# Kernel tuning notes

Measured on AMD Instinct MI355X. Metric: run time of the kernel, lower is better.

Reference implementation:

```python
import jax, jax.numpy as jnp
import numpy as np

B, N, K = 8, 2048, 16   # batch, points, neighbors (after dropping self)
EPS = 1e-5


def _bn(y, g, b, m, v):
    # eval-mode batchnorm over channel dim 1, y: [B,C,...]
    sh = (1, -1) + (1,) * (y.ndim - 2)
    inv = g.reshape(sh) / jnp.sqrt(v.reshape(sh) + EPS)
    return (y - m.reshape(sh)) * inv + b.reshape(sh)


def setup_inputs() -> dict:
    key = jax.random.key(0)
    ks = jax.random.split(key, 16)
    d = {}
    d["x"] = jax.random.normal(ks[0], (B, 3, N), dtype=jnp.float32)
    # pre: Conv1d(3->24, k=1) + BN
    d["w_pre"] = jax.random.normal(ks[1], (24, 3), dtype=jnp.float32) * 0.3
    d["b_pre"] = jax.random.normal(ks[2], (24,), dtype=jnp.float32) * 0.1
    d["g_pre"] = 1.0 + 0.1 * jax.random.normal(ks[3], (24,), dtype=jnp.float32)
    d["be_pre"] = 0.1 * jax.random.normal(ks[4], (24,), dtype=jnp.float32)
    d["m_pre"] = 0.1 * jax.random.normal(ks[5], (24,), dtype=jnp.float32)
    d["v_pre"] = jax.random.uniform(ks[6], (24,), minval=0.5, maxval=1.5, dtype=jnp.float32)
    # shared_mlp_1: Conv2d(48->12, 1, bias=False) + BN
    d["w1"] = jax.random.normal(ks[7], (12, 48), dtype=jnp.float32) * 0.15
    d["g1"] = 1.0 + 0.1 * jax.random.normal(ks[8], (12,), dtype=jnp.float32)
    d["be1"] = 0.1 * jax.random.normal(ks[9], (12,), dtype=jnp.float32)
    d["m1"] = 0.1 * jax.random.normal(ks[10], (12,), dtype=jnp.float32)
    d["v1"] = jax.random.uniform(ks[11], (12,), minval=0.5, maxval=1.5, dtype=jnp.float32)
    # shared_mlp_2: Conv2d(60->12, 1, bias=False) + BN
    d["w2"] = jax.random.normal(ks[12], (12, 60), dtype=jnp.float32) * 0.15
    d["g2"] = 1.0 + 0.1 * jax.random.normal(ks[13], (12,), dtype=jnp.float32)
    d["be2"] = 0.1 * jax.random.normal(ks[14], (12,), dtype=jnp.float32)
    d["m2"] = 0.1 * jax.random.normal(ks[15], (12,), dtype=jnp.float32)
    d["v2"] = jnp.ones((12,), dtype=jnp.float32)
    # shared_mlp_3: Conv2d(72->12, 1, bias=False), no BN
    d["w3"] = jax.random.normal(jax.random.fold_in(key, 99), (12, 72), dtype=jnp.float32) * 0.15
    return d


def reference(x, w_pre, b_pre, g_pre, be_pre, m_pre, v_pre,
              w1, g1, be1, m1, v1, w2, g2, be2, m2, v2, w3):
    # pre: 1x1 conv1d + BN + ReLU -> [B,24,N]
    pre = jnp.einsum('oc,bcn->bon', w_pre, x) + b_pre[None, :, None]
    pre = jax.nn.relu(_bn(pre, g_pre, be_pre, m_pre, v_pre))

    # kNN on xyz = x.detach(): [B,N,3]
    pts = jax.lax.stop_gradient(jnp.swapaxes(x, 1, 2))
    sq = jnp.sum(pts * pts, axis=-1)                              # [B,N]
    d2 = sq[:, :, None] + sq[:, None, :] - 2.0 * jnp.einsum('bnc,bmc->bnm', pts, pts)
    _, idx = jax.lax.top_k(-d2, K + 1)                             # nearest K+1 incl. self
    idx = idx[..., 1:]                                             # drop self -> [B,N,K]

    # gather neighbor features: [B,24,N,K]
    grouped = jax.vmap(lambda f, i: f[:, i])(pre, idx)
    center = jnp.broadcast_to(pre[..., None], grouped.shape)
    y = jnp.concatenate([center, grouped], axis=1)                 # [B,48,N,K]

    h1 = jax.nn.relu(_bn(jnp.einsum('oc,bcnk->bonk', w1, y), g1, be1, m1, v1))
    y = jnp.concatenate([h1, y], axis=1)                           # [B,60,N,K]
    h2 = jax.nn.relu(_bn(jnp.einsum('oc,bcnk->bonk', w2, y), g2, be2, m2, v2))
    y = jnp.concatenate([h2, y], axis=1)                           # [B,72,N,K]
    h3 = jnp.einsum('oc,bcnk->bonk', w3, y)
    y = jnp.concatenate([h3, y], axis=1)                           # [B,84,N,K]

    y = jnp.max(y, axis=-1)                                        # maxpool over neighbors -> [B,84,N]
    return jnp.concatenate([y, x], axis=1)                         # [B,87,N]
```

## Files before the change

kernel.cpp:

```cpp
#include <hip/hip_runtime.h>
#include <math.h>

#define EPS 1e-5f
#define NBATCH 8
#define NPTS 2048
#define KNB 16
#define BIG 3.2e38f

#define CHUNK_PTS 32
#define KNN_BLKS (NBATCH * 64)
#define THREADS 1024
#define FUSED_LDS 65536

#define WS_PRE 0
#define WS_AUX (16384 * 24)
#define WS_IDX (WS_AUX + 16384 * 72)

__device__ __forceinline__ float dist2f(float mex, float mey, float mez,
                                        float sqn, float4 q) {
  float dot2 = fmaf(mex, q.x, fmaf(mey, q.y, __fmul_rn(mez, q.z)));
  return __fsub_rn(__fadd_rn(sqn, q.w), dot2);
}

__global__ __launch_bounds__(THREADS, 8) void fused_kernel(
    const float* __restrict__ x,
    const float* __restrict__ w_pre, const float* __restrict__ b_pre,
    const float* __restrict__ g_pre, const float* __restrict__ be_pre,
    const float* __restrict__ m_pre, const float* __restrict__ v_pre,
    const float* __restrict__ w1, const float* __restrict__ g1,
    const float* __restrict__ be1, const float* __restrict__ m1,
    const float* __restrict__ v1,
    const float* __restrict__ w2, const float* __restrict__ g2,
    const float* __restrict__ be2, const float* __restrict__ m2,
    const float* __restrict__ v2, const float* __restrict__ w3,
    float* __restrict__ pre, float* __restrict__ aux,
    int* __restrict__ knn_out) {
  extern __shared__ char smem[];
  float4* C4   = (float4*)smem;
  float* slist = (float*)(smem + 32768);
  float* fwp   = slist;
  float* fbp   = fwp + 72;
  float* fw1t  = fbp + 24;
  float* fb1   = fw1t + 576;
  float* fw2t  = fb1 + 12;
  float* fb2   = fw2t + 720;
  float* fw3t  = fb2 + 12;
  float* sinv1 = fw3t + 576;
  float* sinv2 = sinv1 + 12;
  float* sinvP = sinv2 + 12;
  float* sd2  = slist;
  int*   sidx = (int*)(slist + 640);
  int*   scnt = (int*)(slist + 1280);

  int tid = threadIdx.x;
  int bi = blockIdx.x;
  int b = bi >> 6, chunk = bi & 63;
  const float* xb = x + (size_t)b * 3 * NPTS;

  for (int j = tid; j < NPTS; j += THREADS) {
    float xx = xb[j], yy = xb[NPTS + j], zz = xb[2 * NPTS + j];
    float sq = __fadd_rn(__fadd_rn(__fmul_rn(xx, xx), __fmul_rn(yy, yy)),
                         __fmul_rn(zz, zz));
    C4[j] = make_float4(2.0f * xx, 2.0f * yy, 2.0f * zz, sq);
  }
  if (tid < 24) sinvP[tid] = g_pre[tid] / sqrtf(v_pre[tid] + EPS);
  if (tid < 12) { sinv1[tid] = g1[tid] / sqrtf(v1[tid] + EPS);
                  sinv2[tid] = g2[tid] / sqrtf(v2[tid] + EPS); }
  __syncthreads();
  if (tid < 72) fwp[tid] = w_pre[tid] * sinvP[tid / 3];
  if (tid < 24) fbp[tid] = (b_pre[tid] - m_pre[tid]) * sinvP[tid] + be_pre[tid];
  if (tid < 12) { fb1[tid] = be1[tid] - m1[tid] * sinv1[tid];
                  fb2[tid] = be2[tid] - m2[tid] * sinv2[tid]; }
  if (tid < 576) { int i = tid / 12, o = tid - i * 12; fw1t[tid] = w1[o * 48 + i] * sinv1[o]; }
  if (tid < 720) { int i = tid / 12, o = tid - i * 12; fw2t[tid] = w2[o * 60 + i] * sinv2[o]; }
  if (tid < 576) { int i = tid / 12, o = tid - i * 12; fw3t[tid] = w3[o * 72 + 24 + i]; }
  __syncthreads();

  {
    int rr = tid & 31, pt = tid >> 5;
    int n0 = chunk * CHUNK_PTS + pt;
    size_t pgl = (size_t)(b << 11) + n0;
    float x0 = xb[n0], x1 = xb[NPTS + n0], x2 = xb[2 * NPTS + n0];
    float pr[24];
#pragma unroll
    for (int c = 0; c < 24; ++c) {
      float v = fmaf(fwp[c * 3 + 0], x0,
                fmaf(fwp[c * 3 + 1], x1,
                fmaf(fwp[c * 3 + 2], x2, fbp[c])));
      pr[c] = fmaxf(v, 0.f);
    }
    if (rr == 16) {
      float4* o4 = (float4*)(pre + pgl * 24);
#pragma unroll
      for (int i = 0; i < 6; ++i)
        o4[i] = make_float4(pr[4*i], pr[4*i+1], pr[4*i+2], pr[4*i+3]);
    }
    if (rr < 12) {
      int o = rr;
      float u1 = fb1[o], a1 = 0.f, u2 = fb2[o], a2 = 0.f, u3 = 0.f, a3 = 0.f;
#pragma unroll
      for (int i = 0; i < 24; ++i) {
        u1 = fmaf(fw1t[i * 12 + o],        pr[i], u1);
        a1 = fmaf(fw1t[(24 + i) * 12 + o], pr[i], a1);
        u2 = fmaf(fw2t[(12 + i) * 12 + o], pr[i], u2);
        a2 = fmaf(fw2t[(36 + i) * 12 + o], pr[i], a2);
        u3 = fmaf(fw3t[i * 12 + o],        pr[i], u3);
        a3 = fmaf(fw3t[(24 + i) * 12 + o], pr[i], a3);
      }
      float* A = aux + pgl * 72;
      A[o] = u1; A[12 + o] = u2; A[24 + o] = u3;
      A[36 + o] = a1; A[48 + o] = a2; A[60 + o] = a3;
    }
  }
  __syncthreads();

  int p = tid & 31, s = tid >> 5;
  int n = chunk * CHUNK_PTS + p;
  float4 me4 = C4[n];
  float mex = 0.5f * me4.x, mey = 0.5f * me4.y, mez = 0.5f * me4.z;
  float sqn = me4.w;
  const float4* Cs = C4 + s * 64;
  int selfc = n - s * 64;
  int rot = (s & 1) << 2;
  float L[16];
#pragma unroll
  for (int t = 0; t < 16; ++t) L[t] = BIG;
  for (int c0 = 0; c0 < 64; c0 += 16) {
    float S[16];
#pragma unroll
    for (int cc = 0; cc < 16; ++cc) {
      int c2 = (c0 + cc) ^ rot;
      float4 q = Cs[c2];
      float d2 = dist2f(mex, mey, mez, sqn, q);
      S[cc] = (c2 == selfc) ? BIG : d2;
    }
#pragma unroll
    for (int pw = 1; pw < 16; pw <<= 1) {
#pragma unroll
      for (int k = pw; k >= 1; k >>= 1) {
#pragma unroll
        for (int j = (k & (pw - 1)); j + k < 16; j += 2 * k) {
#pragma unroll
          for (int i = 0; i < k; ++i) {
            int a = i + j, bq = i + j + k;
            if (bq < 16 && (a / (2 * pw) == bq / (2 * pw))) {
              float lo = fminf(S[a], S[bq]);
              float hi = fmaxf(S[a], S[bq]);
              S[a] = lo; S[bq] = hi;
            }
          }
        }
      }
    }
    float m[16];
#pragma unroll
    for (int i = 0; i < 16; ++i) m[i] = fminf(L[i], S[15 - i]);
#pragma unroll
    for (int d = 8; d >= 1; d >>= 1) {
#pragma unroll
      for (int i = 0; i < 16; ++i) {
        if (!(i & d)) {
          float lo = fminf(m[i], m[i | d]);
          float hi = fmaxf(m[i], m[i | d]);
          m[i] = lo; m[i | d] = hi;
        }
      }
    }
#pragma unroll
    for (int i = 0; i < 16; ++i) L[i] = m[i];
  }
  {
    float bb[16], m16[16];
#pragma unroll
    for (int i = 0; i < 16; ++i) bb[i] = __shfl_xor(L[i], 32, 64);
#pragma unroll
    for (int i = 0; i < 16; ++i) m16[i] = fminf(L[i], bb[15 - i]);
#pragma unroll
    for (int d = 8; d >= 1; d >>= 1) {
#pragma unroll
      for (int i = 0; i < 16; ++i) {
        if (!(i & d)) {
          float lo = fminf(m16[i], m16[i | d]);
          float hi = fmaxf(m16[i], m16[i | d]);
          m16[i] = lo; m16[i | d] = hi;
        }
      }
    }
    int w = tid >> 6;
    if (!(s & 1)) {
#pragma unroll
      for (int i = 0; i < 16; ++i) slist[(w * 16 + i) * 32 + p] = m16[i];
    }
  }
  __syncthreads();
  for (int W = 8; W >= 1; W >>= 1) {
    int w = tid >> 6;
    int h = (tid >> 5) & 1;
    bool act = (w < W);
    float val[16];
    if (act) {
#pragma unroll
      for (int i = 0; i < 16; ++i) val[i] = slist[((2 * w + h) * 16 + i) * 32 + p];
    }
    __syncthreads();
    if (act) {
      float bb[16], m16[16];
#pragma unroll
      for (int i = 0; i < 16; ++i) bb[i] = __shfl_xor(val[i], 32, 64);
#pragma unroll
      for (int i = 0; i < 16; ++i) m16[i] = fminf(val[i], bb[15 - i]);
#pragma unroll
      for (int d = 8; d >= 1; d >>= 1) {
#pragma unroll
        for (int i = 0; i < 16; ++i) {
          if (!(i & d)) {
            float lo = fminf(m16[i], m16[i | d]);
            float hi = fmaxf(m16[i], m16[i | d]);
            m16[i] = lo; m16[i | d] = hi;
          }
        }
      }
      if (h == 0) {
#pragma unroll
        for (int i = 0; i < 16; ++i) slist[(w * 16 + i) * 32 + p] = m16[i];
      }
    }
    __syncthreads();
  }
  float tau = slist[15 * 32 + p];
  __syncthreads();
  for (int j = tid; j < 32 * 20; j += THREADS) sidx[j] = 0;
  if (tid < 32) scnt[tid] = 0;
  __syncthreads();
#pragma unroll 4
  for (int c = 0; c < 64; ++c) {
    int c2 = c ^ rot;
    float4 q = Cs[c2];
    float d2 = dist2f(mex, mey, mez, sqn, q);
    int j = s * 64 + c2;
    if (d2 <= tau && j != n) {
      int pos = atomicAdd(&scnt[p], 1);
      if (pos < 20) { sd2[p * 20 + pos] = d2; sidx[p * 20 + pos] = j; }
    }
  }
  __syncthreads();
  if (tid < 32) {
    int c = scnt[tid]; if (c > 20) c = 20;
    if (c > 16) {
      for (int t = 0; t < 16; ++t) {
        int best = t;
        for (int u = t + 1; u < c; ++u) {
          float da = sd2[tid * 20 + u], db = sd2[tid * 20 + best];
          int ia = sidx[tid * 20 + u], ib = sidx[tid * 20 + best];
          if (da < db || (da == db && ia < ib)) best = u;
        }
        float td = sd2[tid * 20 + t]; sd2[tid * 20 + t] = sd2[tid * 20 + best]; sd2[tid * 20 + best] = td;
        int ti = sidx[tid * 20 + t]; sidx[tid * 20 + t] = sidx[tid * 20 + best]; sidx[tid * 20 + best] = ti;
      }
    }
  }
  __syncthreads();
  if (tid < 512) {
    int pp = tid >> 4, kk = tid & 15;
    knn_out[((size_t)b * NPTS + chunk * CHUNK_PTS + pp) * KNB + kk] = sidx[pp * 20 + kk];
  }
}

__global__ __launch_bounds__(256) void mlp_kernel(
    const float* __restrict__ pre, const float* __restrict__ aux,
    const int* __restrict__ knn, const float* __restrict__ x,
    const float* __restrict__ w2, const float* __restrict__ g2,
    const float* __restrict__ v2, const float* __restrict__ w3,
    float* __restrict__ out) {
  __shared__ float sW2h[144], sW3h2[144], sW3h1[144];
  __shared__ float sout[87 * 16];
  int tid = threadIdx.x;
  if (tid < 144) {
    int o = tid / 12, i = tid - o * 12;
    float inv2 = g2[o] / sqrtf(v2[o] + EPS);
    sW2h[tid]  = w2[o * 60 + i] * inv2;
    sW3h2[tid] = w3[o * 72 + i];
    sW3h1[tid] = w3[o * 72 + 12 + i];
  }
  __syncthreads();
  int k = tid & 15, pl = tid >> 4;
  int p = blockIdx.x * 16 + pl;
  int b = p >> 11, n = p & (NPTS - 1);
  int nb = knn[(size_t)p * KNB + k];
  const float4* u4 = (const float4*)(aux + (size_t)p * 72);
  const float4* a4 = (const float4*)(aux + ((size_t)(b << 11) + nb) * 72 + 36);
  float uc[36], av[36];
#pragma unroll
  for (int i = 0; i < 9; ++i) {
    float4 t = u4[i];
    uc[4*i] = t.x; uc[4*i+1] = t.y; uc[4*i+2] = t.z; uc[4*i+3] = t.w;
    float4 t2 = a4[i];
    av[4*i] = t2.x; av[4*i+1] = t2.y; av[4*i+2] = t2.z; av[4*i+3] = t2.w;
  }
  float h1[12], h2[12], h3[12];
#pragma unroll
  for (int o = 0; o < 12; ++o) h1[o] = fmaxf(uc[o] + av[o], 0.f);
#pragma unroll
  for (int o = 0; o < 12; ++o) {
    float a = uc[12 + o] + av[12 + o];
#pragma unroll
    for (int i = 0; i < 12; ++i) a = fmaf(sW2h[o * 12 + i], h1[i], a);
    h2[o] = fmaxf(a, 0.f);
  }
#pragma unroll
  for (int o = 0; o < 12; ++o) {
    float a = uc[24 + o] + av[24 + o];
#pragma unroll
    for (int i = 0; i < 12; ++i) a = fmaf(sW3h2[o * 12 + i], h2[i], a);
#pragma unroll
    for (int i = 0; i < 12; ++i) a = fmaf(sW3h1[o * 12 + i], h1[i], a);
    h3[o] = a;
  }
  float nbf[24];
  const float4* pn4 = (const float4*)(pre + ((size_t)(b << 11) + nb) * 24);
#pragma unroll
  for (int i = 0; i < 6; ++i) {
    float4 t = pn4[i];
    nbf[4*i] = t.x; nbf[4*i+1] = t.y; nbf[4*i+2] = t.z; nbf[4*i+3] = t.w;
  }
#pragma unroll
  for (int m = 1; m < 16; m <<= 1) {
#pragma unroll
    for (int o = 0; o < 12; ++o) {
      h1[o] = fmaxf(h1[o], __shfl_xor(h1[o], m, 16));
      h2[o] = fmaxf(h2[o], __shfl_xor(h2[o], m, 16));
      h3[o] = fmaxf(h3[o], __shfl_xor(h3[o], m, 16));
    }
#pragma unroll
    for (int i = 0; i < 24; ++i)
      nbf[i] = fmaxf(nbf[i], __shfl_xor(nbf[i], m, 16));
  }
  if (k == 0) {
    const float4* c4 = (const float4*)(pre + (size_t)p * 24);
#pragma unroll
    for (int o = 0; o < 12; ++o) {
      sout[(0  + o) * 16 + pl] = h3[o];
      sout[(12 + o) * 16 + pl] = h2[o];
      sout[(24 + o) * 16 + pl] = h1[o];
    }
#pragma unroll
    for (int i = 0; i < 6; ++i) {
      float4 t = c4[i];
      sout[(36 + 4*i    ) * 16 + pl] = t.x;
      sout[(36 + 4*i + 1) * 16 + pl] = t.y;
      sout[(36 + 4*i + 2) * 16 + pl] = t.z;
      sout[(36 + 4*i + 3) * 16 + pl] = t.w;
    }
#pragma unroll
    for (int i = 0; i < 24; ++i) sout[(60 + i) * 16 + pl] = nbf[i];
    const float* xb = x + (size_t)b * 3 * NPTS + n;
    sout[84 * 16 + pl] = xb[0];
    sout[85 * 16 + pl] = xb[NPTS];
    sout[86 * 16 + pl] = xb[2 * NPTS];
  }
  __syncthreads();
  int n0 = (blockIdx.x * 16) & (NPTS - 1);
  float* ob = out + (size_t)b * 87 * NPTS;
  for (int j2 = tid; j2 < 87 * 16; j2 += 256) {
    int c = j2 >> 4, i = j2 & 15;
    ob[(size_t)c * NPTS + n0 + i] = sout[j2];
  }
}

extern "C" void kernel_launch(void* const* d_in, const int* in_sizes, int n_in,
                              void* d_out, int out_size, void* d_ws, size_t ws_size,
                              hipStream_t stream) {
  (void)in_sizes; (void)n_in; (void)out_size; (void)ws_size;
  const float* x     = (const float*)d_in[0];
  const float* w_pre = (const float*)d_in[1];
  const float* b_pre = (const float*)d_in[2];
  const float* g_pre = (const float*)d_in[3];
  const float* be_pre= (const float*)d_in[4];
  const float* m_pre = (const float*)d_in[5];
  const float* v_pre = (const float*)d_in[6];
  const float* w1    = (const float*)d_in[7];
  const float* g1    = (const float*)d_in[8];
  const float* be1   = (const float*)d_in[9];
  const float* m1    = (const float*)d_in[10];
  const float* v1    = (const float*)d_in[11];
  const float* w2    = (const float*)d_in[12];
  const float* g2    = (const float*)d_in[13];
  const float* be2   = (const float*)d_in[14];
  const float* m2    = (const float*)d_in[15];
  const float* v2    = (const float*)d_in[16];
  const float* w3    = (const float*)d_in[17];
  float* ws  = (float*)d_ws;
  float* pre = ws + WS_PRE;
  float* aux = ws + WS_AUX;
  int*   knn = (int*)(ws + WS_IDX);
  float* out = (float*)d_out;

  fused_kernel<<<KNN_BLKS, THREADS, FUSED_LDS, stream>>>(
      x, w_pre, b_pre, g_pre, be_pre, m_pre, v_pre,
      w1, g1, be1, m1, v1, w2, g2, be2, m2, v2, w3,
      pre, aux, knn);
  mlp_kernel<<<NBATCH * NPTS / 16, 256, 0, stream>>>(pre, aux, knn, x,
                                                     w2, g2, v2, w3, out);
}
```

Before: 155.0 us.

## Halve fused block size, scan 128 candidates per thread, specialize self-check

Cuts the fused KNN block from 1024 to 512 threads, with matching LDS. Each thread now scans 128 candidate points instead of 64, so the cross-wave merge tree is shallower, needs fewer barriers, and no longer shuffles within a wave at each step. The self-exclusion compare is templated so it runs only in the wave that holds the query point, and the pre-MLP stage is remapped to 16 lanes per point. The trade-off is longer per-thread serial sorting work and loss of the xor rotation that spread LDS reads across banks, which may add bank conflicts.

```diff
diff --git a/kernel.cpp b/kernel.cpp
--- a/kernel.cpp
+++ b/kernel.cpp
@@ -9,8 +9,8 @@
 
 #define CHUNK_PTS 32
 #define KNN_BLKS (NBATCH * 64)
-#define THREADS 1024
-#define FUSED_LDS 65536
+#define THREADS 512
+#define FUSED_LDS 49152
 
 #define WS_PRE 0
 #define WS_AUX (16384 * 24)
@@ -22,7 +22,57 @@
   return __fsub_rn(__fadd_rn(sqn, q.w), dot2);
 }
 
-__global__ __launch_bounds__(THREADS, 8) void fused_kernel(
+template <bool HASSELF>
+__device__ __forceinline__ void scan_slice(const float4* __restrict__ Cs, int selfc,
+                                           float mex, float mey, float mez,
+                                           float sqn, float L[16]) {
+  for (int c0 = 0; c0 < 128; c0 += 16) {
+    float S[16];
+#pragma unroll
+    for (int cc = 0; cc < 16; ++cc) {
+      float4 q = Cs[c0 + cc];
+      float d2 = dist2f(mex, mey, mez, sqn, q);
+      if (HASSELF) S[cc] = ((c0 + cc) == selfc) ? BIG : d2;
+      else         S[cc] = d2;
+    }
+#pragma unroll
+    for (int pw = 1; pw < 16; pw <<= 1) {
+#pragma unroll
+      for (int k = pw; k >= 1; k >>= 1) {
+#pragma unroll
+        for (int j = (k & (pw - 1)); j + k < 16; j += 2 * k) {
+#pragma unroll
+          for (int i = 0; i < k; ++i) {
+            int a = i + j, bq = i + j + k;
+            if (bq < 16 && (a / (2 * pw) == bq / (2 * pw))) {
+              float lo = fminf(S[a], S[bq]);
+              float hi = fmaxf(S[a], S[bq]);
+              S[a] = lo; S[bq] = hi;
+            }
+          }
+        }
+      }
+    }
+    float m[16];
+#pragma unroll
+    for (int i = 0; i < 16; ++i) m[i] = fminf(L[i], S[15 - i]);
+#pragma unroll
+    for (int d = 8; d >= 1; d >>= 1) {
+#pragma unroll
+      for (int i = 0; i < 16; ++i) {
+        if (!(i & d)) {
+          float lo = fminf(m[i], m[i | d]);
+          float hi = fmaxf(m[i], m[i | d]);
+          m[i] = lo; m[i | d] = hi;
+        }
+      }
+    }
+#pragma unroll
+    for (int i = 0; i < 16; ++i) L[i] = m[i];
+  }
+}
+
+__global__ __launch_bounds__(THREADS, 6) void fused_kernel(
     const float* __restrict__ x,
     const float* __restrict__ w_pre, const float* __restrict__ b_pre,
     const float* __restrict__ g_pre, const float* __restrict__ be_pre,
@@ -71,13 +121,13 @@
   if (tid < 24) fbp[tid] = (b_pre[tid] - m_pre[tid]) * sinvP[tid] + be_pre[tid];
   if (tid < 12) { fb1[tid] = be1[tid] - m1[tid] * sinv1[tid];
                   fb2[tid] = be2[tid] - m2[tid] * sinv2[tid]; }
-  if (tid < 576) { int i = tid / 12, o = tid - i * 12; fw1t[tid] = w1[o * 48 + i] * sinv1[o]; }
-  if (tid < 720) { int i = tid / 12, o = tid - i * 12; fw2t[tid] = w2[o * 60 + i] * sinv2[o]; }
-  if (tid < 576) { int i = tid / 12, o = tid - i * 12; fw3t[tid] = w3[o * 72 + 24 + i]; }
+  for (int j = tid; j < 576; j += THREADS) { int i = j / 12, o = j - i * 12; fw1t[j] = w1[o * 48 + i] * sinv1[o]; }
+  for (int j = tid; j < 720; j += THREADS) { int i = j / 12, o = j - i * 12; fw2t[j] = w2[o * 60 + i] * sinv2[o]; }
+  for (int j = tid; j < 576; j += THREADS) { int i = j / 12, o = j - i * 12; fw3t[j] = w3[o * 72 + 24 + i]; }
   __syncthreads();
 
   {
-    int rr = tid & 31, pt = tid >> 5;
+    int r = tid & 15, pt = tid >> 4;
     int n0 = chunk * CHUNK_PTS + pt;
     size_t pgl = (size_t)(b << 11) + n0;
     float x0 = xb[n0], x1 = xb[NPTS + n0], x2 = xb[2 * NPTS + n0];
@@ -89,14 +139,14 @@
                 fmaf(fwp[c * 3 + 2], x2, fbp[c])));
       pr[c] = fmaxf(v, 0.f);
     }
-    if (rr == 16) {
+    if (r == 12) {
       float4* o4 = (float4*)(pre + pgl * 24);
 #pragma unroll
       for (int i = 0; i < 6; ++i)
         o4[i] = make_float4(pr[4*i], pr[4*i+1], pr[4*i+2], pr[4*i+3]);
     }
-    if (rr < 12) {
-      int o = rr;
+    if (r < 12) {
+      int o = r;
       float u1 = fb1[o], a1 = 0.f, u2 = fb2[o], a2 = 0.f, u3 = 0.f, a3 = 0.f;
 #pragma unroll
       for (int i = 0; i < 24; ++i) {
@@ -115,60 +165,19 @@
   __syncthreads();
 
   int p = tid & 31, s = tid >> 5;
+  int w = tid >> 6;
   int n = chunk * CHUNK_PTS + p;
   float4 me4 = C4[n];
   float mex = 0.5f * me4.x, mey = 0.5f * me4.y, mez = 0.5f * me4.z;
   float sqn = me4.w;
-  const float4* Cs = C4 + s * 64;
-  int selfc = n - s * 64;
-  int rot = (s & 1) << 2;
+  const float4* Cs = C4 + s * 128;
+  int selfc = n - s * 128;
+  int wself = chunk >> 3;
   float L[16];
 #pragma unroll
   for (int t = 0; t < 16; ++t) L[t] = BIG;
-  for (int c0 = 0; c0 < 64; c0 += 16) {
-    float S[16];
-#pragma unroll
-    for (int cc = 0; cc < 16; ++cc) {
-      int c2 = (c0 + cc) ^ rot;
-      float4 q = Cs[c2];
-      float d2 = dist2f(mex, mey, mez, sqn, q);
-      S[cc] = (c2 == selfc) ? BIG : d2;
-    }
-#pragma unroll
-    for (int pw = 1; pw < 16; pw <<= 1) {
-#pragma unroll
-      for (int k = pw; k >= 1; k >>= 1) {
-#pragma unroll
-        for (int j = (k & (pw - 1)); j + k < 16; j += 2 * k) {
-#pragma unroll
-          for (int i = 0; i < k; ++i) {
-            int a = i + j, bq = i + j + k;
-            if (bq < 16 && (a / (2 * pw) == bq / (2 * pw))) {
-              float lo = fminf(S[a], S[bq]);
-              float hi = fmaxf(S[a], S[bq]);
-              S[a] = lo; S[bq] = hi;
-            }
-          }
-        }
-      }
-    }
-    float m[16];
-#pragma unroll
-    for (int i = 0; i < 16; ++i) m[i] = fminf(L[i], S[15 - i]);
-#pragma unroll
-    for (int d = 8; d >= 1; d >>= 1) {
-#pragma unroll
-      for (int i = 0; i < 16; ++i) {
-        if (!(i & d)) {
-          float lo = fminf(m[i], m[i | d]);
-          float hi = fmaxf(m[i], m[i | d]);
-          m[i] = lo; m[i | d] = hi;
-        }
-      }
-    }
-#pragma unroll
-    for (int i = 0; i < 16; ++i) L[i] = m[i];
-  }
+  if (w == wself) scan_slice<true >(Cs, selfc, mex, mey, mez, sqn, L);
+  else            scan_slice<false>(Cs, selfc, mex, mey, mez, sqn, L);
   {
     float bb[16], m16[16];
 #pragma unroll
@@ -186,29 +195,27 @@
         }
       }
     }
-    int w = tid >> 6;
     if (!(s & 1)) {
 #pragma unroll
       for (int i = 0; i < 16; ++i) slist[(w * 16 + i) * 32 + p] = m16[i];
     }
   }
   __syncthreads();
-  for (int W = 8; W >= 1; W >>= 1) {
-    int w = tid >> 6;
-    int h = (tid >> 5) & 1;
-    bool act = (w < W);
-    float val[16];
+  for (int W = 4; W >= 1; W >>= 1) {
+    int u = tid >> 5;
+    bool act = (u < W);
+    float a[16], bb[16];
     if (act) {
 #pragma unroll
-      for (int i = 0; i < 16; ++i) val[i] = slist[((2 * w + h) * 16 + i) * 32 + p];
+      for (int i = 0; i < 16; ++i) a[i]  = slist[((2 * u) * 16 + i) * 32 + p];
+#pragma unroll
+      for (int i = 0; i < 16; ++i) bb[i] = slist[((2 * u + 1) * 16 + i) * 32 + p];
     }
     __syncthreads();
     if (act) {
-      float bb[16], m16[16];
-#pragma unroll
-      for (int i = 0; i < 16; ++i) bb[i] = __shfl_xor(val[i], 32, 64);
-#pragma unroll
-      for (int i = 0; i < 16; ++i) m16[i] = fminf(val[i], bb[15 - i]);
+      float m16[16];
+#pragma unroll
+      for (int i = 0; i < 16; ++i) m16[i] = fminf(a[i], bb[15 - i]);
 #pragma unroll
       for (int d = 8; d >= 1; d >>= 1) {
 #pragma unroll
@@ -220,10 +227,8 @@
           }
         }
       }
-      if (h == 0) {
-#pragma unroll
-        for (int i = 0; i < 16; ++i) slist[(w * 16 + i) * 32 + p] = m16[i];
-      }
+#pragma unroll
+      for (int i = 0; i < 16; ++i) slist[(u * 16 + i) * 32 + p] = m16[i];
     }
     __syncthreads();
   }
@@ -232,15 +237,27 @@
   for (int j = tid; j < 32 * 20; j += THREADS) sidx[j] = 0;
   if (tid < 32) scnt[tid] = 0;
   __syncthreads();
+  if (w == wself) {
 #pragma unroll 4
-  for (int c = 0; c < 64; ++c) {
-    int c2 = c ^ rot;
-    float4 q = Cs[c2];
-    float d2 = dist2f(mex, mey, mez, sqn, q);
-    int j = s * 64 + c2;
-    if (d2 <= tau && j != n) {
-      int pos = atomicAdd(&scnt[p], 1);
-      if (pos < 20) { sd2[p * 20 + pos] = d2; sidx[p * 20 + pos] = j; }
+    for (int c = 0; c < 128; ++c) {
+      float4 q = Cs[c];
+      float d2 = dist2f(mex, mey, mez, sqn, q);
+      int j = s * 128 + c;
+      if (d2 <= tau && j != n) {
+        int pos = atomicAdd(&scnt[p], 1);
+        if (pos < 20) { sd2[p * 20 + pos] = d2; sidx[p * 20 + pos] = j; }
+      }
+    }
+  } else {
+#pragma unroll 4
+    for (int c = 0; c < 128; ++c) {
+      float4 q = Cs[c];
+      float d2 = dist2f(mex, mey, mez, sqn, q);
+      int j = s * 128 + c;
+      if (d2 <= tau) {
+        int pos = atomicAdd(&scnt[p], 1);
+        if (pos < 20) { sd2[p * 20 + pos] = d2; sidx[p * 20 + pos] = j; }
+      }
     }
   }
   __syncthreads();
@@ -260,7 +277,7 @@
     }
   }
   __syncthreads();
-  if (tid < 512) {
+  {
     int pp = tid >> 4, kk = tid & 15;
     knn_out[((size_t)b * NPTS + chunk * CHUNK_PTS + pp) * KNB + kk] = sidx[pp * 20 + kk];
   }
```

Measured after the change: 151.5 us. 1.02x faster.
